# Kernel tuning notes

Measured on AMD Instinct MI355X. Metric: run time of the kernel, lower is better.

The kernel has to match this reference:

```python
import jax, jax.numpy as jnp
import numpy as np

M = 10000      # spans with antecedents
KMAX = 30      # max antecedents per span
N = 12000      # total candidate spans (rows of g_i)
GDIM = 512     # span embedding dim
DDIM, GEDIM, SDIM = 20, 20, 20  # distance / genre / speaker embed dims
HID = 150      # Score hidden dim
GIJ = 3 * GDIM + DDIM + GEDIM + SDIM  # 1596
NDIST, NGENRE, NSPK = 10, 7, 3


def setup_inputs() -> dict:
    rng = np.random.default_rng(0)
    lengths = rng.integers(1, KMAX + 1, size=M)           # antecedents per span
    P = int(lengths.sum())
    seg_ids = np.repeat(np.arange(1, M + 1), lengths).astype(np.int32)  # segment 0 is the leading empty split
    pos_in_seg = np.concatenate([np.arange(l) for l in lengths]).astype(np.int32)
    seg_lengths = np.concatenate([[0], lengths]).astype(np.int32)        # [S], S = M+1
    mention_ids = rng.integers(0, N, size=P).astype(np.int32)
    antecedent_ids = rng.integers(0, N, size=P).astype(np.int32)
    dist_idx = rng.integers(0, NDIST, size=P).astype(np.int32)
    genre_idx = rng.integers(0, NGENRE, size=P).astype(np.int32)
    speaker_idx = rng.integers(0, NSPK, size=P).astype(np.int32)

    ks = jax.random.split(jax.random.key(0), 12)
    sc = lambda d: 1.0 / np.sqrt(d)
    return {
        'g_i': jax.random.normal(ks[0], (N, GDIM), jnp.float32),
        'mention_scores': jax.random.normal(ks[1], (N, 1), jnp.float32),
        'dist_emb': jax.random.normal(ks[2], (NDIST, DDIM), jnp.float32),
        'genre_emb': jax.random.normal(ks[3], (NGENRE, GEDIM), jnp.float32),
        'speaker_emb': jax.random.normal(ks[4], (NSPK, SDIM), jnp.float32),
        'W1': jax.random.normal(ks[5], (GIJ, HID), jnp.float32) * sc(GIJ),
        'b1': jnp.zeros((HID,), jnp.float32),
        'W2': jax.random.normal(ks[6], (HID, HID), jnp.float32) * sc(HID),
        'b2': jnp.zeros((HID,), jnp.float32),
        'W3': jax.random.normal(ks[7], (HID, 1), jnp.float32) * sc(HID),
        'b3': jnp.zeros((1,), jnp.float32),
        'mention_ids': jnp.asarray(mention_ids),
        'antecedent_ids': jnp.asarray(antecedent_ids),
        'dist_idx': jnp.asarray(dist_idx),
        'genre_idx': jnp.asarray(genre_idx),
        'speaker_idx': jnp.asarray(speaker_idx),
        'seg_ids': jnp.asarray(seg_ids),
        'pos_in_seg': jnp.asarray(pos_in_seg),
        'seg_lengths': jnp.asarray(seg_lengths),
    }


def reference(g_i, mention_scores, dist_emb, genre_emb, speaker_emb,
              W1, b1, W2, b2, W3, b3,
              mention_ids, antecedent_ids, dist_idx, genre_idx, speaker_idx,
              seg_ids, pos_in_seg, seg_lengths):
    # phi = cat(distance, genre, speaker) side features, [P, 60]
    phi = jnp.concatenate([dist_emb[dist_idx], genre_emb[genre_idx], speaker_emb[speaker_idx]], axis=1)
    i_g = g_i[mention_ids]      # [P, GDIM] irregular gather
    j_g = g_i[antecedent_ids]   # [P, GDIM]
    pairs = jnp.concatenate([i_g, j_g, i_g * j_g, phi], axis=1)  # [P, GIJ]
    # 3-layer MLP scorer (dropout is identity at inference)
    h = jax.nn.relu(pairs @ W1 + b1)
    h = jax.nn.relu(h @ W2 + b2)
    s_ij = (h @ W3 + b3)[:, 0]  # [P]
    coref = mention_scores[mention_ids, 0] + mention_scores[antecedent_ids, 0] + s_ij  # [P]
    # variable-length segment softmax with epsilon=0 appended, padded with 1000
    S = seg_lengths.shape[0]
    dense = jnp.full((S, KMAX + 1), -jnp.inf, jnp.float32)
    dense = dense.at[seg_ids, pos_in_seg].set(coref)
    dense = dense.at[jnp.arange(S), seg_lengths].set(0.0)  # epsilon slot
    probs = jax.nn.softmax(dense, axis=1)  # -inf slots -> 0
    col = jnp.arange(KMAX + 1)
    probs = jnp.where(col[None, :] > seg_lengths[:, None], 1000.0, probs)  # pad value 1000
    return probs  # [S, KMAX+1]
```

## Files before the change

### kernel.cpp

```cpp
#include <hip/hip_runtime.h>
#include <stdint.h>

#define GDIM   512
#define HID    150
#define HIDP   160
#define NROWS  12000
#define KP1    31
#define BMP    128
#define BMF    128

typedef __attribute__((ext_vector_type(4))) float f32x4;
typedef __attribute__((ext_vector_type(2))) float f32x2;
typedef long i64;

__device__ __forceinline__ unsigned short f2bf(float x){
    unsigned int u = __float_as_uint(x);
    return (unsigned short)((u + 0x7fffu + ((u >> 16) & 1u)) >> 16);
}
__device__ __forceinline__ float bf2f(unsigned short u){
    return __uint_as_float(((unsigned int)u) << 16);
}
__device__ __forceinline__ i64 u2l(uint2 v){ return __builtin_bit_cast(i64, v); }
__device__ __forceinline__ f32x4 mfma8(i64 a, i64 b, f32x4 c){
    return __builtin_amdgcn_mfma_f32_16x16x32_fp8_fp8(a, b, c, 0, 0, 0);
}
__device__ __forceinline__ uint2 f8mulpk(uint2 m, uint2 a){
    f32x2 m0 = __builtin_amdgcn_cvt_pk_f32_fp8(m.x, false);
    f32x2 m1 = __builtin_amdgcn_cvt_pk_f32_fp8(m.x, true);
    f32x2 m2 = __builtin_amdgcn_cvt_pk_f32_fp8(m.y, false);
    f32x2 m3 = __builtin_amdgcn_cvt_pk_f32_fp8(m.y, true);
    f32x2 a0 = __builtin_amdgcn_cvt_pk_f32_fp8(a.x, false);
    f32x2 a1 = __builtin_amdgcn_cvt_pk_f32_fp8(a.x, true);
    f32x2 a2 = __builtin_amdgcn_cvt_pk_f32_fp8(a.y, false);
    f32x2 a3 = __builtin_amdgcn_cvt_pk_f32_fp8(a.y, true);
    unsigned int r0 = 0, r1 = 0;
    r0 = __builtin_amdgcn_cvt_pk_fp8_f32(m0[0]*a0[0], m0[1]*a0[1], r0, false);
    r0 = __builtin_amdgcn_cvt_pk_fp8_f32(m1[0]*a1[0], m1[1]*a1[1], r0, true);
    r1 = __builtin_amdgcn_cvt_pk_fp8_f32(m2[0]*a2[0], m2[1]*a2[1], r1, false);
    r1 = __builtin_amdgcn_cvt_pk_fp8_f32(m3[0]*a3[0], m3[1]*a3[1], r1, true);
    return (uint2){r0, r1};
}
__device__ __forceinline__ void glds16(const void* g, void* l){
    __builtin_amdgcn_global_load_lds(
        (const __attribute__((address_space(1))) unsigned int*)g,
        (__attribute__((address_space(3))) unsigned int*)l, 16, 0, 0);
}

__global__ void k_prep0(const float* __restrict__ g, unsigned char* __restrict__ g8,
                        int* __restrict__ hist, int4* __restrict__ recs,
                        const float* __restrict__ W1, unsigned char* __restrict__ W18,
                        const float* __restrict__ W2, unsigned char* __restrict__ W28,
                        const float* __restrict__ de, const float* __restrict__ ge,
                        const float* __restrict__ se, const float* __restrict__ b1,
                        const float* __restrict__ W3, const float* __restrict__ b2,
                        unsigned short* __restrict__ PhiW,
                        float* __restrict__ w3p, float* __restrict__ b2p, int P){
    int i = blockIdx.x * blockDim.x + threadIdx.x;
    if (i < NROWS) hist[i] = 0;
    if (i < BMF) recs[P + i] = (int4){0, 0, (int)0x80000000, 0};
    if (i < 30720){
        int s = i / 10240, r = i % 10240;
        int n = r >> 6, gi = r & 63;
        int gdst = gi ^ (n & 7);
        int k0 = s * 512 + gi * 8;
        float x[8];
        #pragma unroll
        for (int e = 0; e < 8; e++) x[e] = (n < HID) ? W1[(size_t)(k0 + e) * HID + n] : 0.f;
        unsigned int d0 = 0, d1 = 0;
        d0 = __builtin_amdgcn_cvt_pk_fp8_f32(x[0], x[1], d0, false);
        d0 = __builtin_amdgcn_cvt_pk_fp8_f32(x[2], x[3], d0, true);
        d1 = __builtin_amdgcn_cvt_pk_fp8_f32(x[4], x[5], d1, false);
        d1 = __builtin_amdgcn_cvt_pk_fp8_f32(x[6], x[7], d1, true);
        *reinterpret_cast<uint2*>(W18 + (size_t)s * 81920 + n * 512 + gdst * 8) = (uint2){d0, d1};
    }
    if (i < 6912){
        int n2 = i / 42, kd = (i % 42) * 4;
        float y[4];
        #pragma unroll
        for (int e = 0; e < 4; e++){
            int k = kd + e;
            y[e] = (n2 < HID && k < HID) ? W2[(size_t)k * HID + n2] : 0.f;
        }
        unsigned int d = 0;
        d = __builtin_amdgcn_cvt_pk_fp8_f32(y[0], y[1], d, false);
        d = __builtin_amdgcn_cvt_pk_fp8_f32(y[2], y[3], d, true);
        reinterpret_cast<unsigned int*>(W28)[i] = d;
    }
    if (i < NROWS * 32){
        int lh = i & 3, kt = (i >> 2) & 7, row = i >> 5;
        const float* src = g + (size_t)row * 512 + kt * 64 + lh * 8;
        float4 x0 = *reinterpret_cast<const float4*>(src);
        float4 x1 = *reinterpret_cast<const float4*>(src + 4);
        float4 x2 = *reinterpret_cast<const float4*>(src + 32);
        float4 x3 = *reinterpret_cast<const float4*>(src + 36);
        uint4 o; unsigned int d;
        d = 0; d = __builtin_amdgcn_cvt_pk_fp8_f32(x0.x, x0.y, d, false);
        d = __builtin_amdgcn_cvt_pk_fp8_f32(x0.z, x0.w, d, true);  o.x = d;
        d = 0; d = __builtin_amdgcn_cvt_pk_fp8_f32(x1.x, x1.y, d, false);
        d = __builtin_amdgcn_cvt_pk_fp8_f32(x1.z, x1.w, d, true);  o.y = d;
        d = 0; d = __builtin_amdgcn_cvt_pk_fp8_f32(x2.x, x2.y, d, false);
        d = __builtin_amdgcn_cvt_pk_fp8_f32(x2.z, x2.w, d, true);  o.z = d;
        d = 0; d = __builtin_amdgcn_cvt_pk_fp8_f32(x3.x, x3.y, d, false);
        d = __builtin_amdgcn_cvt_pk_fp8_f32(x3.z, x3.w, d, true);  o.w = d;
        *reinterpret_cast<uint4*>(g8 + (size_t)row * 512 + kt * 64 + lh * 16) = o;
    } else if (i < NROWS * 32 + 33600){
        int j = i - NROWS * 32;
        int c = j / HIDP, h = j - c * HIDP;
        int si = c % 3, gi2 = (c / 3) % 7, di = c / 21;
        float acc = 0.f;
        if (h < HID){
            acc = b1[h];
            #pragma unroll
            for (int dd = 0; dd < 20; dd++) acc += de[di*20 + dd] * W1[(size_t)(1536 + dd) * HID + h];
            #pragma unroll
            for (int dd = 0; dd < 20; dd++) acc += ge[gi2*20 + dd] * W1[(size_t)(1556 + dd) * HID + h];
            #pragma unroll
            for (int dd = 0; dd < 20; dd++) acc += se[si*20 + dd] * W1[(size_t)(1576 + dd) * HID + h];
        }
        PhiW[c * HIDP + h] = f2bf(acc);
    } else if (i < NROWS * 32 + 33600 + HIDP){
        int h = i - NROWS * 32 - 33600;
        w3p[h] = (h < HID) ? W3[h] : 0.f;
        b2p[h] = (h < HID) ? b2[h] : 0.f;
    }
}

__global__ void k_hist(const int* __restrict__ mid, int* __restrict__ hist, int P){
    int p = blockIdx.x * blockDim.x + threadIdx.x;
    if (p < P) atomicAdd(&hist[mid[p]], 1);
}
__global__ void k_scan(const int* __restrict__ hist, int* __restrict__ offsw, int nb){
    __shared__ int part[1024];
    int t = threadIdx.x;
    int chunk = (nb + 1023) / 1024;
    int lo = t * chunk, hi = lo + chunk; if (hi > nb) hi = nb;
    int s = 0;
    for (int b = lo; b < hi; b++) s += hist[b];
    part[t] = s;
    __syncthreads();
    for (int d = 1; d < 1024; d <<= 1){
        int v = (t >= d) ? part[t - d] : 0;
        __syncthreads();
        part[t] += v;
        __syncthreads();
    }
    int run = part[t] - s;
    for (int b = lo; b < hi; b++){ offsw[b] = run; run += hist[b]; }
}
__global__ void k_scatter(const int* __restrict__ mident, const int* __restrict__ antid,
                          const int* __restrict__ di, const int* __restrict__ gi, const int* __restrict__ si,
                          const int* __restrict__ seg, const int* __restrict__ pos, const float* __restrict__ ms,
                          int* __restrict__ offsw, int4* __restrict__ recs, int P){
    int p = blockIdx.x * blockDim.x + threadIdx.x;
    if (p >= P) return;
    int m = mident[p], a = antid[p];
    int idx = atomicAdd(&offsw[m], 1);
    int combo = (di[p] * 7 + gi[p]) * 3 + si[p];
    int meta = (combo << 19) | (seg[p] << 5) | pos[p];
    int4 r; r.x = m; r.y = a; r.z = meta; r.w = __float_as_int(ms[m] + ms[a]);
    recs[idx] = r;
}

__global__ __launch_bounds__(256) void k_proj(const unsigned char* __restrict__ g8,
                                              const unsigned char* __restrict__ W18,
                                              unsigned char* __restrict__ out){
    __shared__ __align__(16) char smem[81920];
    const unsigned char* Wt = W18 + (size_t)blockIdx.y * 81920;
    unsigned char* outh = out + (size_t)blockIdx.y * NROWS * HIDP;
    int tid = threadIdx.x, lane = tid & 63, w = tid >> 6;
    int l15 = lane & 15, lh = lane >> 4;
    int swz8 = (l15 & 7) << 3;
    int row0 = blockIdx.x * BMP;

    int r0 = row0 + 32*w + l15;       int r0c = (r0 < NROWS) ? r0 : NROWS - 1;
    int r1 = r0 + 16;                 int r1c = (r1 < NROWS) ? r1 : NROWS - 1;
    const unsigned char* gp0 = g8 + (size_t)r0c * GDIM + lh * 16;
    const unsigned char* gp1 = g8 + (size_t)r1c * GDIM + lh * 16;

    #pragma unroll
    for (int i = 0; i < 20; i++){
        int c = w * 20 + i;
        glds16(Wt + c * 1024 + lane * 16, smem + c * 1024);
    }

    f32x4 acc1[10][2];
    #pragma unroll
    for (int t = 0; t < 10; t++){ acc1[t][0] = (f32x4){0,0,0,0}; acc1[t][1] = (f32x4){0,0,0,0}; }

#define LOADAP(kt, R) do{ \
    R[0] = *reinterpret_cast<const uint4*>(gp0 + (kt)*64); \
    R[1] = *reinterpret_cast<const uint4*>(gp1 + (kt)*64); \
}while(0)
#define COMPP(kt, R) do{ \
    i64 a00 = u2l((uint2){R[0].x, R[0].y}), a01 = u2l((uint2){R[0].z, R[0].w}); \
    i64 a10 = u2l((uint2){R[1].x, R[1].y}), a11 = u2l((uint2){R[1].z, R[1].w}); \
    _Pragma("unroll") \
    for (int t = 0; t < 10; t++){ \
        int rowb = (t*16 + l15) * 512; \
        i64 b0 = *reinterpret_cast<const i64*>(&smem[rowb + (((kt)*64 +  0 + lh*8) ^ swz8)]); \
        i64 b1 = *reinterpret_cast<const i64*>(&smem[rowb + (((kt)*64 + 32 + lh*8) ^ swz8)]); \
        acc1[t][0] = mfma8(b0, a00, acc1[t][0]); \
        acc1[t][1] = mfma8(b0, a10, acc1[t][1]); \
        acc1[t][0] = mfma8(b1, a01, acc1[t][0]); \
        acc1[t][1] = mfma8(b1, a11, acc1[t][1]); \
    } \
}while(0)

    uint4 A0[2], A1[2], A2[2];
    LOADAP(0, A0); LOADAP(1, A1);
    asm volatile("s_waitcnt vmcnt(4)" ::: "memory");
    __builtin_amdgcn_s_barrier();

    LOADAP(2, A2); COMPP(0, A0);
    LOADAP(3, A0); COMPP(1, A1);
    LOADAP(4, A1); COMPP(2, A2);
    LOADAP(5, A2); COMPP(3, A0);
    LOADAP(6, A0); COMPP(4, A1);
    LOADAP(7, A1); COMPP(5, A2);
    COMPP(6, A0);
    COMPP(7, A1);
#undef LOADAP
#undef COMPP

    #pragma unroll
    for (int rf = 0; rf < 2; rf++){
        int row = row0 + 32*w + 16*rf + l15;
        if (row < NROWS){
            #pragma unroll
            for (int t = 0; t < 10; t++){
                f32x4 a = acc1[t][rf];
                unsigned int dw = 0;
                dw = __builtin_amdgcn_cvt_pk_fp8_f32(a[0], a[1], dw, false);
                dw = __builtin_amdgcn_cvt_pk_fp8_f32(a[2], a[3], dw, true);
                *reinterpret_cast<unsigned int*>(outh + (size_t)row * HIDP + 16*t + 4*lh) = dw;
            }
        }
    }
}

__global__ __launch_bounds__(256) void k_fused(
    const unsigned char* __restrict__ g8,
    const unsigned char* __restrict__ W1c8, const unsigned char* __restrict__ W28,
    const unsigned short* __restrict__ PhiW, const unsigned char* __restrict__ Am,
    const unsigned char* __restrict__ Aa,
    const float* __restrict__ w3p, const float* __restrict__ b2p, const float* __restrict__ b3,
    const int4* __restrict__ recs,
    float* __restrict__ dense)
{
    __shared__ __align__(16) char smem[81920];
    int tid = threadIdx.x, lane = tid & 63, w = tid >> 6;
    int l15 = lane & 15, lh = lane >> 4;
    int swz8 = (l15 & 7) << 3;

    int nwg = gridDim.x, orig = blockIdx.x, bid = orig;
    if (nwg >= 8){
        int q = nwg >> 3, r = nwg & 7;
        int xcd = orig & 7, lid = orig >> 3;
        bid = (xcd < r ? xcd * (q + 1) : r * (q + 1) + (xcd - r) * q) + lid;
    }
    int p0 = bid * BMF;

    int4 rec0 = recs[p0 + 32*w + l15];
    int4 rec1 = recs[p0 + 32*w + 16 + l15];

    const unsigned char* gm0 = g8 + (size_t)rec0.x * GDIM + lh * 16;
    const unsigned char* ga0 = g8 + (size_t)rec0.y * GDIM + lh * 16;
    const unsigned char* gm1 = g8 + (size_t)rec1.x * GDIM + lh * 16;
    const unsigned char* ga1 = g8 + (size_t)rec1.y * GDIM + lh * 16;

    #pragma unroll
    for (int i = 0; i < 20; i++){
        int c = w * 20 + i;
        glds16(W1c8 + c * 1024 + lane * 16, smem + c * 1024);
    }

    f32x4 acc1[10][2];
    #pragma unroll
    for (int t = 0; t < 10; t++){ acc1[t][0] = (f32x4){0,0,0,0}; acc1[t][1] = (f32x4){0,0,0,0}; }

#define LOADAF(kt, R) do{ \
    R[0] = *reinterpret_cast<const uint4*>(gm0 + (kt)*64); \
    R[1] = *reinterpret_cast<const uint4*>(ga0 + (kt)*64); \
    R[2] = *reinterpret_cast<const uint4*>(gm1 + (kt)*64); \
    R[3] = *reinterpret_cast<const uint4*>(ga1 + (kt)*64); \
}while(0)
#define COMPF(kt, R) do{ \
    uint2 p00 = f8mulpk((uint2){R[0].x, R[0].y}, (uint2){R[1].x, R[1].y}); \
    uint2 p01 = f8mulpk((uint2){R[0].z, R[0].w}, (uint2){R[1].z, R[1].w}); \
    uint2 p10 = f8mulpk((uint2){R[2].x, R[2].y}, (uint2){R[3].x, R[3].y}); \
    uint2 p11 = f8mulpk((uint2){R[2].z, R[2].w}, (uint2){R[3].z, R[3].w}); \
    i64 lp00 = u2l(p00), lp01 = u2l(p01), lp10 = u2l(p10), lp11 = u2l(p11); \
    _Pragma("unroll") \
    for (int t = 0; t < 10; t++){ \
        int rowb = (t*16 + l15) * 512; \
        i64 b0 = *reinterpret_cast<const i64*>(&smem[rowb + (((kt)*64 +  0 + lh*8) ^ swz8)]); \
        i64 b1 = *reinterpret_cast<const i64*>(&smem[rowb + (((kt)*64 + 32 + lh*8) ^ swz8)]); \
        acc1[t][0] = mfma8(b0, lp00, acc1[t][0]); \
        acc1[t][1] = mfma8(b0, lp10, acc1[t][1]); \
        acc1[t][0] = mfma8(b1, lp01, acc1[t][0]); \
        acc1[t][1] = mfma8(b1, lp11, acc1[t][1]); \
    } \
}while(0)

    uint4 A0[4], A1[4], A2[4];
    LOADAF(0, A0); LOADAF(1, A1);
    asm volatile("s_waitcnt vmcnt(8)" ::: "memory");
    __builtin_amdgcn_s_barrier();

    LOADAF(2, A2); COMPF(0, A0);
    LOADAF(3, A0); COMPF(1, A1);
    LOADAF(4, A1); COMPF(2, A2);
    LOADAF(5, A2); COMPF(3, A0);
    LOADAF(6, A0); COMPF(4, A1);
    LOADAF(7, A1); COMPF(5, A2);
    COMPF(6, A0);
    COMPF(7, A1);
#undef LOADAF
#undef COMPF

    asm volatile("s_waitcnt lgkmcnt(0)" ::: "memory");
    __builtin_amdgcn_s_barrier();

    #pragma unroll
    for (int i = 0; i < 7; i++){
        int c = w * 7 + i;
        if (c < 27) glds16(W28 + c * 1024 + lane * 16, smem + 21504 + c * 1024);
    }

    #pragma unroll
    for (int rf = 0; rf < 2; rf++){
        int4 rc = rf ? rec1 : rec0;
        int pr = 32*w + 16*rf + l15;
        const unsigned char* amp = Am + (size_t)rc.x * HIDP;
        const unsigned char* aap = Aa + (size_t)rc.y * HIDP;
        int combo = (rc.z >> 19) & 0xFF;
        const unsigned short* php = PhiW + (size_t)combo * HIDP;
        char* h1row = smem + pr * 168;
        #pragma unroll
        for (int t = 0; t < 10; t++){
            int h0 = 16*t + 4*lh;
            unsigned int amd = *reinterpret_cast<const unsigned int*>(amp + h0);
            unsigned int aad = *reinterpret_cast<const unsigned int*>(aap + h0);
            ushort4 ph4 = *reinterpret_cast<const ushort4*>(php + h0);
            f32x2 amL = __builtin_amdgcn_cvt_pk_f32_fp8(amd, false);
            f32x2 amH = __builtin_amdgcn_cvt_pk_f32_fp8(amd, true);
            f32x2 aaL = __builtin_amdgcn_cvt_pk_f32_fp8(aad, false);
            f32x2 aaH = __builtin_amdgcn_cvt_pk_f32_fp8(aad, true);
            f32x4 a = acc1[t][rf];
            float v0 = fmaxf(a[0] + amL[0] + aaL[0] + bf2f(ph4.x), 0.f);
            float v1 = fmaxf(a[1] + amL[1] + aaL[1] + bf2f(ph4.y), 0.f);
            float v2 = fmaxf(a[2] + amH[0] + aaH[0] + bf2f(ph4.z), 0.f);
            float v3 = fmaxf(a[3] + amH[1] + aaH[1] + bf2f(ph4.w), 0.f);
            unsigned int dw = 0;
            dw = __builtin_amdgcn_cvt_pk_fp8_f32(v0, v1, dw, false);
            dw = __builtin_amdgcn_cvt_pk_fp8_f32(v2, v3, dw, true);
            *reinterpret_cast<unsigned int*>(h1row + h0) = dw;
        }
    }

    asm volatile("s_waitcnt vmcnt(0) lgkmcnt(0)" ::: "memory");
    __builtin_amdgcn_s_barrier();

    f32x4 acc2[10][2];
    #pragma unroll
    for (int t = 0; t < 10; t++){ acc2[t][0] = (f32x4){0,0,0,0}; acc2[t][1] = (f32x4){0,0,0,0}; }
    const char* w2b = smem + 21504;
    #pragma unroll
    for (int k2 = 0; k2 < 5; k2++){
        i64 h0f = *reinterpret_cast<const i64*>(smem + (32*w + l15)      * 168 + k2*32 + lh*8);
        i64 h1f = *reinterpret_cast<const i64*>(smem + (32*w + 16 + l15) * 168 + k2*32 + lh*8);
        #pragma unroll
        for (int t = 0; t < 10; t++){
            i64 wf = *reinterpret_cast<const i64*>(w2b + (16*t + l15) * 168 + k2*32 + lh*8);
            acc2[t][0] = mfma8(wf, h0f, acc2[t][0]);
            acc2[t][1] = mfma8(wf, h1f, acc2[t][1]);
        }
    }

    float b3v = b3[0];
    #pragma unroll
    for (int rf = 0; rf < 2; rf++){
        int4 rc = rf ? rec1 : rec0;
        float s = 0.f;
        #pragma unroll
        for (int t = 0; t < 10; t++){
            f32x4 w3v = *reinterpret_cast<const f32x4*>(w3p + 16*t + 4*lh);
            f32x4 b2v = *reinterpret_cast<const f32x4*>(b2p + 16*t + 4*lh);
            f32x4 a = acc2[t][rf];
            s += fmaxf(a[0] + b2v[0], 0.f) * w3v[0];
            s += fmaxf(a[1] + b2v[1], 0.f) * w3v[1];
            s += fmaxf(a[2] + b2v[2], 0.f) * w3v[2];
            s += fmaxf(a[3] + b2v[3], 0.f) * w3v[3];
        }
        s += __shfl_xor(s, 16);
        s += __shfl_xor(s, 32);
        if (!(rc.z & 0x80000000) && lh == 0){
            float val = s + b3v + __int_as_float(rc.w);
            dense[(size_t)((rc.z >> 5) & 0x3FFF) * KP1 + (rc.z & 31)] = val;
        }
    }
}

__global__ void k_softmax(const float* __restrict__ dense, const int* __restrict__ seg_lengths,
                          float* __restrict__ out, int S){
    int wid = threadIdx.x >> 6, lane = threadIdx.x & 63;
    int s = blockIdx.x * 4 + wid;
    if (s >= S) return;
    int len = seg_lengths[s];
    float ninf = -__builtin_inff();
    float val = ninf;
    if (lane < KP1) val = (lane < len) ? dense[(size_t)s * KP1 + lane] : ((lane == len) ? 0.f : ninf);
    float m = val;
    #pragma unroll
    for (int msk = 1; msk < 64; msk <<= 1) m = fmaxf(m, __shfl_xor(m, msk));
    float e = expf(val - m);
    float sum = e;
    #pragma unroll
    for (int msk = 1; msk < 64; msk <<= 1) sum += __shfl_xor(sum, msk);
    if (lane < KP1) out[(size_t)s * KP1 + lane] = (lane > len) ? 1000.f : (e / sum);
}

extern "C" void kernel_launch(void* const* d_in, const int* in_sizes, int n_in,
                              void* d_out, int out_size, void* d_ws, size_t ws_size,
                              hipStream_t stream){
    const float* g_i        = (const float*)d_in[0];
    const float* ms         = (const float*)d_in[1];
    const float* dist_emb   = (const float*)d_in[2];
    const float* genre_emb  = (const float*)d_in[3];
    const float* spk_emb    = (const float*)d_in[4];
    const float* W1         = (const float*)d_in[5];
    const float* b1         = (const float*)d_in[6];
    const float* W2         = (const float*)d_in[7];
    const float* b2         = (const float*)d_in[8];
    const float* W3         = (const float*)d_in[9];
    const float* b3         = (const float*)d_in[10];
    const int* mention_ids  = (const int*)d_in[11];
    const int* antecedent_ids = (const int*)d_in[12];
    const int* dist_idx     = (const int*)d_in[13];
    const int* genre_idx    = (const int*)d_in[14];
    const int* spk_idx      = (const int*)d_in[15];
    const int* seg_ids      = (const int*)d_in[16];
    const int* pos_in_seg   = (const int*)d_in[17];
    const int* seg_lengths  = (const int*)d_in[18];
    int P = in_sizes[11];
    int S = in_sizes[18];

    char* ws = (char*)d_ws;
    unsigned char* W18   = (unsigned char*)(ws + 0);
    unsigned char* W28   = (unsigned char*)(ws + 245760);
    unsigned short* PhiW = (unsigned short*)(ws + 273408);
    float* w3pad         = (float*)(ws + 340608);
    float* b2pad         = (float*)(ws + 341248);
    unsigned char* g8    = (unsigned char*)(ws + 341888);
    unsigned char* Am8   = (unsigned char*)(ws + 6485888);
    unsigned char* Aa8   = (unsigned char*)(ws + 8405888);
    int* hist            = (int*)(ws + 10325888);
    int* offsw           = (int*)(ws + 10373888);
    int4* recs           = (int4*)(ws + 10421888);
    float* dense         = (float*)(ws + 13000192);

    int prep_threads = NROWS * 32 + 33600 + HIDP;
    k_prep0<<<(prep_threads + 255)/256, 256, 0, stream>>>(g_i, g8, hist, recs, W1, W18, W2, W28,
        dist_emb, genre_emb, spk_emb, b1, W3, b2, PhiW, w3pad, b2pad, P);
    k_hist<<<(P + 255)/256, 256, 0, stream>>>(mention_ids, hist, P);
    k_scan<<<1, 1024, 0, stream>>>(hist, offsw, NROWS);
    k_scatter<<<(P + 255)/256, 256, 0, stream>>>(mention_ids, antecedent_ids, dist_idx, genre_idx,
        spk_idx, seg_ids, pos_in_seg, ms, offsw, recs, P);

    k_proj<<<dim3((NROWS + BMP - 1)/BMP, 2), 256, 0, stream>>>(g8, W18, Am8);

    k_fused<<<(P + BMF - 1)/BMF, 256, 0, stream>>>(g8, W18 + 2*81920, W28, PhiW,
        Am8, Aa8, w3pad, b2pad, b3, recs, dense);

    k_softmax<<<(S + 3)/4, 256, 0, stream>>>(dense, seg_lengths, (float*)d_out, S);
}
```

Before: 115.2 us.

## Restructure GEMM prefetch pipelines, add MFMA priority hints and occupancy bound

The projection kernel swaps its 3-deep register ring for a simple double-buffered loop. It now waits for the weight LDS fill before issuing any row loads. The fused kernel moves its weight-fill wait ahead of the gather loads and wraps the MFMA loops in s_setprio to favour matrix issue across waves. It also sets launch_bounds(256,2) to target two workgroups per CU. These changes lose some load/compute overlap at the start of each loop, and the occupancy bound may push registers to spill.

```diff
diff --git a/kernel.cpp b/kernel.cpp
--- a/kernel.cpp
+++ b/kernel.cpp
@@ -187,40 +187,34 @@
     #pragma unroll
     for (int t = 0; t < 10; t++){ acc1[t][0] = (f32x4){0,0,0,0}; acc1[t][1] = (f32x4){0,0,0,0}; }
 
-#define LOADAP(kt, R) do{ \
-    R[0] = *reinterpret_cast<const uint4*>(gp0 + (kt)*64); \
-    R[1] = *reinterpret_cast<const uint4*>(gp1 + (kt)*64); \
-}while(0)
-#define COMPP(kt, R) do{ \
-    i64 a00 = u2l((uint2){R[0].x, R[0].y}), a01 = u2l((uint2){R[0].z, R[0].w}); \
-    i64 a10 = u2l((uint2){R[1].x, R[1].y}), a11 = u2l((uint2){R[1].z, R[1].w}); \
-    _Pragma("unroll") \
-    for (int t = 0; t < 10; t++){ \
-        int rowb = (t*16 + l15) * 512; \
-        i64 b0 = *reinterpret_cast<const i64*>(&smem[rowb + (((kt)*64 +  0 + lh*8) ^ swz8)]); \
-        i64 b1 = *reinterpret_cast<const i64*>(&smem[rowb + (((kt)*64 + 32 + lh*8) ^ swz8)]); \
-        acc1[t][0] = mfma8(b0, a00, acc1[t][0]); \
-        acc1[t][1] = mfma8(b0, a10, acc1[t][1]); \
-        acc1[t][0] = mfma8(b1, a01, acc1[t][0]); \
-        acc1[t][1] = mfma8(b1, a11, acc1[t][1]); \
-    } \
-}while(0)
-
-    uint4 A0[2], A1[2], A2[2];
-    LOADAP(0, A0); LOADAP(1, A1);
-    asm volatile("s_waitcnt vmcnt(4)" ::: "memory");
+    asm volatile("s_waitcnt vmcnt(0)" ::: "memory");
     __builtin_amdgcn_s_barrier();
 
-    LOADAP(2, A2); COMPP(0, A0);
-    LOADAP(3, A0); COMPP(1, A1);
-    LOADAP(4, A1); COMPP(2, A2);
-    LOADAP(5, A2); COMPP(3, A0);
-    LOADAP(6, A0); COMPP(4, A1);
-    LOADAP(7, A1); COMPP(5, A2);
-    COMPP(6, A0);
-    COMPP(7, A1);
-#undef LOADAP
-#undef COMPP
+    uint4 R0 = *reinterpret_cast<const uint4*>(gp0);
+    uint4 R1 = *reinterpret_cast<const uint4*>(gp1);
+    #pragma unroll
+    for (int kt = 0; kt < 8; kt++){
+        uint4 N0, N1;
+        if (kt < 7){
+            N0 = *reinterpret_cast<const uint4*>(gp0 + (kt+1)*64);
+            N1 = *reinterpret_cast<const uint4*>(gp1 + (kt+1)*64);
+        }
+        i64 a00 = u2l((uint2){R0.x, R0.y}), a01 = u2l((uint2){R0.z, R0.w});
+        i64 a10 = u2l((uint2){R1.x, R1.y}), a11 = u2l((uint2){R1.z, R1.w});
+        __builtin_amdgcn_s_setprio(1);
+        #pragma unroll
+        for (int t = 0; t < 10; t++){
+            int rowb = (t*16 + l15) * 512;
+            i64 b0 = *reinterpret_cast<const i64*>(&smem[rowb + ((kt*64 +  0 + lh*8) ^ swz8)]);
+            i64 b1 = *reinterpret_cast<const i64*>(&smem[rowb + ((kt*64 + 32 + lh*8) ^ swz8)]);
+            acc1[t][0] = mfma8(b0, a00, acc1[t][0]);
+            acc1[t][1] = mfma8(b0, a10, acc1[t][1]);
+            acc1[t][0] = mfma8(b1, a01, acc1[t][0]);
+            acc1[t][1] = mfma8(b1, a11, acc1[t][1]);
+        }
+        __builtin_amdgcn_s_setprio(0);
+        R0 = N0; R1 = N1;
+    }
 
     #pragma unroll
     for (int rf = 0; rf < 2; rf++){
@@ -238,7 +232,7 @@
     }
 }
 
-__global__ __launch_bounds__(256) void k_fused(
+__global__ __launch_bounds__(256, 2) void k_fused(
     const unsigned char* __restrict__ g8,
     const unsigned char* __restrict__ W1c8, const unsigned char* __restrict__ W28,
     const unsigned short* __restrict__ PhiW, const unsigned char* __restrict__ Am,
@@ -278,6 +272,9 @@
     #pragma unroll
     for (int t = 0; t < 10; t++){ acc1[t][0] = (f32x4){0,0,0,0}; acc1[t][1] = (f32x4){0,0,0,0}; }
 
+    asm volatile("s_waitcnt vmcnt(0)" ::: "memory");
+    __builtin_amdgcn_s_barrier();
+
 #define LOADAF(kt, R) do{ \
     R[0] = *reinterpret_cast<const uint4*>(gm0 + (kt)*64); \
     R[1] = *reinterpret_cast<const uint4*>(ga0 + (kt)*64); \
@@ -290,6 +287,7 @@
     uint2 p10 = f8mulpk((uint2){R[2].x, R[2].y}, (uint2){R[3].x, R[3].y}); \
     uint2 p11 = f8mulpk((uint2){R[2].z, R[2].w}, (uint2){R[3].z, R[3].w}); \
     i64 lp00 = u2l(p00), lp01 = u2l(p01), lp10 = u2l(p10), lp11 = u2l(p11); \
+    __builtin_amdgcn_s_setprio(1); \
     _Pragma("unroll") \
     for (int t = 0; t < 10; t++){ \
         int rowb = (t*16 + l15) * 512; \
@@ -300,13 +298,11 @@
         acc1[t][0] = mfma8(b1, lp01, acc1[t][0]); \
         acc1[t][1] = mfma8(b1, lp11, acc1[t][1]); \
     } \
+    __builtin_amdgcn_s_setprio(0); \
 }while(0)
 
     uint4 A0[4], A1[4], A2[4];
     LOADAF(0, A0); LOADAF(1, A1);
-    asm volatile("s_waitcnt vmcnt(8)" ::: "memory");
-    __builtin_amdgcn_s_barrier();
-
     LOADAF(2, A2); COMPF(0, A0);
     LOADAF(3, A0); COMPF(1, A1);
     LOADAF(4, A1); COMPF(2, A2);
@@ -365,6 +361,7 @@
     #pragma unroll
     for (int t = 0; t < 10; t++){ acc2[t][0] = (f32x4){0,0,0,0}; acc2[t][1] = (f32x4){0,0,0,0}; }
     const char* w2b = smem + 21504;
+    __builtin_amdgcn_s_setprio(1);
     #pragma unroll
     for (int k2 = 0; k2 < 5; k2++){
         i64 h0f = *reinterpret_cast<const i64*>(smem + (32*w + l15)      * 168 + k2*32 + lh*8);
@@ -376,6 +373,7 @@
             acc2[t][1] = mfma8(wf, h1f, acc2[t][1]);
         }
     }
+    __builtin_amdgcn_s_setprio(0);
 
     float b3v = b3[0];
     #pragma unroll
```

After: 114.7 us. No clear change (-0.5%).
